# Optimization experiments

Measured on AMD Instinct MI355X. Metric: run time of the kernel, lower is better.

Reference implementation:

```python
import jax, jax.numpy as jnp
import numpy as np
from math import factorial

# ----- hyperparams (mirror init_kwargs) -----
HIDDEN = [(32,0,1),(32,0,-1),(8,1,1),(8,1,-1),(4,2,1),(4,2,-1)]  # (mul, l, parity)
SCALAR = [(32,0,1)]
SH_IRR = [(1,0,1),(1,1,-1),(1,2,1)]  # spherical harmonics 0e+1o+2e
EMB, NUM_RBF, R_MAX, MLP_DIM, D_IN = 32, 16, 10.0, 256, 64
N_NODES, N_EDGES, N_GRAPHS = 2048, 8192, 8
EDGE_FEATS_DIM = NUM_RBF + 2*EMB

def _slices(irs):
    s, o = [], 0
    for m, l, _ in irs:
        s.append(o); o += m*(2*l+1)
    return s

def _su2_cg(j1, j2, j3, m1, m2, m3):
    if m1 + m2 != m3:
        return 0.0
    f = factorial
    pref = ((2*j3+1)*f(j3+j1-j2)*f(j3-j1+j2)*f(j1+j2-j3)/f(j1+j2+j3+1))**0.5
    pref *= (f(j3+m3)*f(j3-m3)*f(j1-m1)*f(j1+m1)*f(j2-m2)*f(j2+m2))**0.5
    s = 0.0
    for k in range(0, j1+j2-j3+1):
        if j1-m1-k < 0 or j2+m2-k < 0 or j3-j2+m1+k < 0 or j3-j1-m2+k < 0:
            continue
        s += (-1.0)**k/(f(k)*f(j1+j2-j3-k)*f(j1-m1-k)*f(j2+m2-k)*f(j3-j2+m1+k)*f(j3-j1-m2+k))
    return pref*s

def _q(l):  # real -> complex change of basis (e3nn convention incl. (-i)^l phase)
    q = np.zeros((2*l+1, 2*l+1), dtype=np.complex128)
    for m in range(-l, 0):
        q[l+m, l+abs(m)] = 2**-0.5
        q[l+m, l-abs(m)] = -1j*2**-0.5
    q[l, l] = 1.0
    for m in range(1, l+1):
        q[l+m, l+abs(m)] = (-1)**m*2**-0.5
        q[l+m, l-abs(m)] = 1j*(-1)**m*2**-0.5
    return (-1j)**l*q

def _real_cg(l1, l2, l3):  # real-basis Clebsch-Gordan, unit Frobenius norm (wigner-3j-like)
    C = np.zeros((2*l1+1, 2*l2+1, 2*l3+1), dtype=np.complex128)
    for m1 in range(-l1, l1+1):
        for m2 in range(-l2, l2+1):
            m3 = m1 + m2
            if abs(m3) <= l3:
                C[l1+m1, l2+m2, l3+m3] = _su2_cg(l1, l2, l3, m1, m2, m3)
    w = np.einsum('ai,bj,ck,abc->ijk', _q(l1), _q(l2), np.conj(_q(l3)), C)
    re, im = np.real(w), np.imag(w)
    w = re if np.linalg.norm(re) >= np.linalg.norm(im) else im
    return (w/np.linalg.norm(w)).astype(np.float32)

_CG = {}
def cg(l1, l2, l3):
    if (l1, l2, l3) not in _CG:
        _CG[(l1, l2, l3)] = jnp.asarray(_real_cg(l1, l2, l3))
    return _CG[(l1, l2, l3)]

def _build_layer(ir_in, ir_out):  # FullyConnectedTensorProduct path enumeration
    si = _slices(ir_in)
    paths, woff, fan = [], 0, [0]*len(ir_out)
    for i1, (m1, l1, p1) in enumerate(ir_in):
        for (_, l2, p2) in SH_IRR:
            for i3, (m3, l3, p3) in enumerate(ir_out):
                if p1*p2 == p3 and abs(l1-l2) <= l3 <= l1+l2:
                    paths.append((si[i1], m1, l1, l2, i3, m3, l3, woff))
                    fan[i3] += m1
                    woff += m1*m3
    return paths, woff, fan, ir_out

L_SPECS = [_build_layer(SCALAR, HIDDEN), _build_layer(HIDDEN, HIDDEN),
           _build_layer(HIDDEN, HIDDEN), _build_layer(HIDDEN, SCALAR)]
W_NUMELS = [s[1] for s in L_SPECS]  # [1408, 4320, 4320, 1408]

def spherical_harmonics(u):  # component-normalized real SH, l=0,1,2, on unit vectors
    xc, yc, zc = u[:, 0], u[:, 1], u[:, 2]
    s3, s15, s5 = 3**0.5, 15**0.5, 5**0.5
    return jnp.stack([jnp.ones_like(xc),
                      s3*yc, s3*zc, s3*xc,
                      s15*xc*yc, s15*yc*zc, s5*0.5*(3*zc*zc-1.0), s15*xc*zc,
                      s15*0.5*(xc*xc-yc*yc)], axis=1)

def tp_messages(x, sh, w, spec):  # per-edge equivariant tensor product with edge-dep weights
    paths, _, fan, ir_out = spec
    E = x.shape[0]
    outs = [jnp.zeros((E, m*(2*l+1)), x.dtype) for m, l, _ in ir_out]
    for (o1, m1, l1, l2, i3, m3, l3, woff) in paths:
        xp = x[:, o1:o1+m1*(2*l1+1)].reshape(E, m1, 2*l1+1)
        shp = sh[:, l2*l2:(l2+1)*(l2+1)]
        wp = w[:, woff:woff+m1*m3].reshape(E, m1, m3)
        alpha = float(np.sqrt((2*l3+1)/fan[i3]))  # component/element path normalization
        y = alpha*jnp.einsum('eui,ej,euv,ijk->evk', xp, shp, wp, cg(l1, l2, l3))
        outs[i3] = outs[i3] + y.reshape(E, -1)
    return jnp.concatenate(outs, axis=1)

def batch_norm(h, ir_out, eps=1e-5):  # e3nn-style equivariant batch norm (train stats, identity affine)
    outs, o = [], 0
    for m, l, _ in ir_out:
        d = m*(2*l+1)
        f = h[:, o:o+d].reshape(-1, m, 2*l+1); o += d
        if l == 0:
            f = f - f.mean(axis=0, keepdims=True)
        norm2 = (f*f).mean(axis=(0, 2), keepdims=True)
        outs.append((f*jax.lax.rsqrt(norm2+eps)).reshape(h.shape[0], -1))
    return jnp.concatenate(outs, axis=1)

def scatter_mean(msg, idx, n):
    s = jax.ops.segment_sum(msg, idx, num_segments=n)
    c = jax.ops.segment_sum(jnp.ones((idx.shape[0], 1), msg.dtype), idx, num_segments=n)
    return s/jnp.maximum(c, 1.0)

def _forward(x, pos, edge_index, batch, emb_w, emb_b, layer_params):
    ei = jnp.concatenate([edge_index, edge_index[::-1]], axis=1)  # to_undirected (both directions)
    src, dst = ei[0], ei[1]
    h = x@emb_w + emb_b  # (N, 32)
    vec = pos[src] - pos[dst]
    lengths = jnp.linalg.norm(vec, axis=-1)
    sh = spherical_harmonics(vec/lengths[:, None])  # (E, 9)
    mu = jnp.linspace(0.0, R_MAX, NUM_RBF)
    sigma = R_MAX/NUM_RBF
    rbf = jnp.exp(-(((lengths[:, None]-mu)/sigma)**2))  # (E, 16)
    for li, (w1, b1, w2, b2) in enumerate(layer_params):
        ef = jnp.concatenate([rbf, h[src, :EMB], h[dst, :EMB]], axis=1)  # (E, 80)
        w = jax.nn.relu(ef@w1 + b1)@w2 + b2  # per-edge TP weights (dropout=eval noop)
        upd = scatter_mean(tp_messages(h[dst], sh, w, L_SPECS[li]), src, N_NODES)
        upd = batch_norm(upd, L_SPECS[li][3])
        d = upd.shape[-1]
        h_res = h[:, :d] if h.shape[-1] >= d else jnp.pad(h, ((0, 0), (0, d-h.shape[-1])))
        h = upd + h_res  # residual with pad/truncate (F.pad semantics)
    graph = jax.ops.segment_sum(h, batch, num_segments=N_GRAPHS)
    return h, graph

def setup_inputs():
    key = jax.random.key(0)
    ks = jax.random.split(key, 32)
    inp = {}
    inp['x'] = jax.random.normal(ks[0], (N_NODES, D_IN), jnp.float32)
    inp['pos'] = 3.0*jax.random.normal(ks[1], (N_NODES, 3), jnp.float32)
    s = jax.random.randint(ks[2], (N_EDGES,), 0, N_NODES)
    d = (s + jax.random.randint(ks[3], (N_EDGES,), 1, N_NODES)) % N_NODES  # no self-loops
    inp['edge_index'] = jnp.stack([s, d]).astype(jnp.int32)
    inp['batch'] = jnp.sort(jax.random.randint(ks[4], (N_NODES,), 0, N_GRAPHS)).astype(jnp.int32)
    inp['emb_w'] = jax.random.normal(ks[5], (D_IN, EMB), jnp.float32)/np.sqrt(D_IN)
    inp['emb_b'] = jnp.zeros((EMB,), jnp.float32)
    k = 6
    for i, wn in enumerate(W_NUMELS):
        inp[f'l{i}_w1'] = jax.random.normal(ks[k], (EDGE_FEATS_DIM, MLP_DIM), jnp.float32)/np.sqrt(EDGE_FEATS_DIM); k += 1
        inp[f'l{i}_b1'] = jnp.zeros((MLP_DIM,), jnp.float32)
        inp[f'l{i}_w2'] = jax.random.normal(ks[k], (MLP_DIM, wn), jnp.float32)/np.sqrt(MLP_DIM); k += 1
        inp[f'l{i}_b2'] = jnp.zeros((wn,), jnp.float32)
    return inp

def reference(x, pos, edge_index, batch, emb_w, emb_b,
              l0_w1, l0_b1, l0_w2, l0_b2, l1_w1, l1_b1, l1_w2, l1_b2,
              l2_w1, l2_b1, l2_w2, l2_b2, l3_w1, l3_b1, l3_w2, l3_b2):
    lp = [(l0_w1, l0_b1, l0_w2, l0_b2), (l1_w1, l1_b1, l1_w2, l1_b2),
          (l2_w1, l2_b1, l2_w2, l2_b2), (l3_w1, l3_b1, l3_w2, l3_b2)]
    return _forward(x, pos, edge_index, batch, emb_w, emb_b, lp)
```

## Files before the change

kernel.cpp:

```cpp
#include <hip/hip_runtime.h>
#include <hip/hip_bf16.h>
#include <math.h>

#define NNODES 2048
#define NEDG   8192
#define E2     16384
#define NGRAPH 8
#define HSTR   152

static const int LD_DIN[4]  = {32,152,152,152};
static const int LD_DOUT[4] = {152,152,152,32};
static const int LD_WN[4]   = {1408,4320,4320,1408};
static const int LD_WNP[4]  = {1408,4352,4352,1408};
static const int LD_NCH[4]  = {88,88,88,32};
static const int LD_RES[4]  = {32,152,152,152};
#define WNP_MAX 4352

#define SLOT_MAX    1088
#define CELL_N      20
#define SEG_S_N     164
#define SEG_ENT_MAX 1024

typedef short bf16x8 __attribute__((ext_vector_type(8)));
typedef float f32x4  __attribute__((ext_vector_type(4)));

constexpr double cfact(int n){ double r=1.0; for(int i=2;i<=n;i++) r*=(double)i; return r; }
constexpr double csqrt(double x){
  if(x<=0.0) return 0.0;
  double g = x>1.0? x:1.0;
  for(int i=0;i<64;i++) g=0.5*(g+x/g);
  return g;
}
constexpr double csu2cg(int j1,int j2,int j3,int m1,int m2,int m3){
  if(m1+m2!=m3) return 0.0;
  double pref = csqrt((double)(2*j3+1)*cfact(j3+j1-j2)*cfact(j3-j1+j2)*cfact(j1+j2-j3)/cfact(j1+j2+j3+1));
  pref *= csqrt(cfact(j3+m3)*cfact(j3-m3)*cfact(j1-m1)*cfact(j1+m1)*cfact(j2-m2)*cfact(j2+m2));
  double s=0.0;
  for(int k=0;k<=j1+j2-j3;k++){
    if(j1-m1-k<0||j2+m2-k<0||j3-j2+m1+k<0||j3-j1-m2+k<0) continue;
    double t=1.0/(cfact(k)*cfact(j1+j2-j3-k)*cfact(j1-m1-k)*cfact(j2+m2-k)*cfact(j3-j2+m1+k)*cfact(j3-j1-m2+k));
    s += (k&1)? -t : t;
  }
  return pref*s;
}
struct QM { double r[25]; double i[25]; };
constexpr QM cqmat(int l){
  QM q{};
  const double inv2=0.7071067811865476;
  for(int m=-l;m<0;m++){
    int am=-m;
    q.r[(l+m)*5+(l+am)] = inv2;
    q.i[(l+m)*5+(l-am)] = -inv2;
  }
  q.r[l*5+l]=1.0;
  for(int m=1;m<=l;m++){
    double sgn=(m&1)? -1.0:1.0;
    q.r[(l+m)*5+(l+m)] = sgn*inv2;
    q.i[(l+m)*5+(l-m)] = sgn*inv2;
  }
  for(int rep=0;rep<l;rep++){
    for(int t=0;t<25;t++){ double a=q.r[t], b=q.i[t]; q.r[t]=b; q.i[t]=-a; }
  }
  return q;
}
struct CGCell { float v[125]; };
constexpr CGCell mkcell(int l1,int l2,int l3){
  CGCell out{};
  int lo = l1>l2? l1-l2 : l2-l1;
  if(l3<lo || l3>l1+l2) return out;
  QM q1=cqmat(l1), q2=cqmat(l2), q3=cqmat(l3);
  int n1=2*l1+1,n2=2*l2+1,n3=2*l3+1;
  double C[125]={};
  for(int a=0;a<n1;a++)for(int b=0;b<n2;b++)for(int c=0;c<n3;c++)
    C[a*25+b*5+c]=csu2cg(l1,l2,l3,a-l1,b-l2,c-l3);
  double wr[125]={}, wi[125]={};
  for(int i=0;i<n1;i++)for(int j=0;j<n2;j++)for(int k=0;k<n3;k++){
    double ar=0.0, ai=0.0;
    for(int a=0;a<n1;a++)for(int b=0;b<n2;b++){
      double p1r=q1.r[a*5+i], p1i=q1.i[a*5+i];
      double p2r=q2.r[b*5+j], p2i=q2.i[b*5+j];
      double pr=p1r*p2r-p1i*p2i, pi=p1r*p2i+p1i*p2r;
      for(int c=0;c<n3;c++){
        double cv=C[a*25+b*5+c]; if(cv==0.0) continue;
        double p3r=q3.r[c*5+k], p3i=-q3.i[c*5+k];
        ar += (pr*p3r-pi*p3i)*cv;
        ai += (pr*p3i+pi*p3r)*cv;
      }
    }
    wr[i*25+j*5+k]=ar; wi[i*25+j*5+k]=ai;
  }
  double sr=0.0, si=0.0;
  for(int t=0;t<125;t++){ sr+=wr[t]*wr[t]; si+=wi[t]*wi[t]; }
  double nr=csqrt(sr), ni=csqrt(si);
  bool use_re = nr>=ni;
  double nn = use_re? nr:ni;
  double inv = (nn>1e-300)? 1.0/nn : 0.0;
  for(int t=0;t<125;t++) out.v[t]=(float)((use_re? wr[t]:wi[t])*inv);
  return out;
}
constexpr CGCell CGc0 =mkcell(0,0,0), CGc1 =mkcell(0,0,1), CGc2 =mkcell(0,0,2);
constexpr CGCell CGc3 =mkcell(0,1,0), CGc4 =mkcell(0,1,1), CGc5 =mkcell(0,1,2);
constexpr CGCell CGc6 =mkcell(0,2,0), CGc7 =mkcell(0,2,1), CGc8 =mkcell(0,2,2);
constexpr CGCell CGc9 =mkcell(1,0,0), CGc10=mkcell(1,0,1), CGc11=mkcell(1,0,2);
constexpr CGCell CGc12=mkcell(1,1,0), CGc13=mkcell(1,1,1), CGc14=mkcell(1,1,2);
constexpr CGCell CGc15=mkcell(1,2,0), CGc16=mkcell(1,2,1), CGc17=mkcell(1,2,2);
constexpr CGCell CGc18=mkcell(2,0,0), CGc19=mkcell(2,0,1), CGc20=mkcell(2,0,2);
constexpr CGCell CGc21=mkcell(2,1,0), CGc22=mkcell(2,1,1), CGc23=mkcell(2,1,2);
constexpr CGCell CGc24=mkcell(2,2,0), CGc25=mkcell(2,2,1), CGc26=mkcell(2,2,2);
__constant__ CGCell g_cg[27] = {
  CGc0,CGc1,CGc2,CGc3,CGc4,CGc5,CGc6,CGc7,CGc8,
  CGc9,CGc10,CGc11,CGc12,CGc13,CGc14,CGc15,CGc16,CGc17,
  CGc18,CGc19,CGc20,CGc21,CGc22,CGc23,CGc24,CGc25,CGc26};

#define MAXP 32
struct LayerSpec {
  int np, zc, wn, nc;
  int x_off[MAXP], m1[MAXP], d1[MAXP], sh_off[MAXP], d2[MAXP], d3[MAXP],
      m3[MAXP], woff[MAXP], out_sl[MAXP], cg_idx[MAXP], zbase[MAXP], cell[MAXP];
  float alpha[MAXP];
  int cellcg[16];
};
constexpr LayerSpec mkspec(int li){
  LayerSpec S{};
  const int IRH[6][3]={{32,0,1},{32,0,-1},{8,1,1},{8,1,-1},{4,2,1},{4,2,-1}};
  const int IRS[1][3]={{32,0,1}};
  const int SH2[3][2]={{0,1},{1,-1},{2,1}};
  const int (*irin)[3]  = (li==0)? IRS: IRH; int nin =(li==0)?1:6;
  const int (*irout)[3] = (li==3)? IRS: IRH; int nout=(li==3)?1:6;
  int si_in[6]={}, si_out[6]={};
  { int o=0; for(int i=0;i<nin;i++){ si_in[i]=o;  o+=irin[i][0]*(2*irin[i][1]+1);} }
  { int o=0; for(int i=0;i<nout;i++){ si_out[i]=o; o+=irout[i][0]*(2*irout[i][1]+1);} }
  int fan[6]={};
  int i3a[MAXP]={};
  int np=0, woff=0, zb=0, nc=0;
  for(int i1=0;i1<nin;i1++){
    int m1=irin[i1][0], l1=irin[i1][1], p1=irin[i1][2];
    for(int s=0;s<3;s++){
      int l2=SH2[s][0], p2=SH2[s][1];
      for(int i3=0;i3<nout;i3++){
        int m3=irout[i3][0], l3=irout[i3][1], p3=irout[i3][2];
        int lo = l1>l2? l1-l2 : l2-l1;
        if(p1*p2==p3 && l3>=lo && l3<=l1+l2){
          S.x_off[np]=si_in[i1]; S.m1[np]=m1; S.d1[np]=2*l1+1;
          S.sh_off[np]=l2*l2; S.d2[np]=2*l2+1; S.d3[np]=2*l3+1;
          S.m3[np]=m3; S.woff[np]=woff; S.out_sl[np]=si_out[i3];
          S.cg_idx[np]=l1*9+l2*3+l3; S.zbase[np]=zb;
          int ci=-1;
          for(int c=0;c<nc;c++) if(S.cellcg[c]==S.cg_idx[np]) ci=c;
          if(ci<0){ S.cellcg[nc]=S.cg_idx[np]; ci=nc++; }
          S.cell[np]=ci; i3a[np]=i3;
          np++;
          fan[i3]+=m1; woff+=m1*m3; zb+=m1*(2*l3+1);
        }
      }
    }
  }
  for(int p=0;p<np;p++)
    S.alpha[p]=(float)csqrt((double)(2*((S.d3[p]-1)/2)+1)/(double)fan[i3a[p]]);
  S.np=np; S.zc=zb; S.wn=woff; S.nc=nc;
  return S;
}
constexpr LayerSpec LS0=mkspec(0), LS1=mkspec(1), LS2=mkspec(2), LS3=mkspec(3);
__constant__ LayerSpec g_spec[4]={LS0,LS1,LS2,LS3};

__global__ __launch_bounds__(256) void build_tables_kernel(
    unsigned* __restrict__ slot_tab, unsigned* __restrict__ cell_tab,
    int* __restrict__ seg_start, unsigned* __restrict__ seg_ent,
    int* __restrict__ perm, float* __restrict__ alpha_col){
  __shared__ int vals[256];
  __shared__ int part[256];
  int tid=threadIdx.x;
  int li=blockIdx.x;
  const LayerSpec& S=g_spec[li];
  int np=S.np, zc=S.zc, nc=S.nc, wn=S.wn;
  for(int c=tid;c<nc;c+=256){
    int cgi=S.cellcg[c];
    int l2=(cgi/3)%3;
    cell_tab[li*CELL_N+c]=(unsigned)cgi | ((unsigned)(l2*l2)<<8) | ((unsigned)(2*l2+1)<<12);
  }
  for(int s=tid;s<zc;s+=256){
    int p=0; while(p+1<np && S.zbase[p+1]<=s) p++;
    int rel=s-S.zbase[p];
    int k=rel/S.m1[p], u=rel-k*S.m1[p];
    slot_tab[li*SLOT_MAX+s]=(unsigned)(S.x_off[p]+u*S.d1[p]) | ((unsigned)k<<9) | ((unsigned)S.cell[p]<<12);
  }
  int* pm=perm+li*WNP_MAX;
  float* ac=alpha_col+li*WNP_MAX;
  for(int j=tid;j<wn;j+=256){
    int p=0; while(p+1<np && S.woff[p+1]<=j) p++;
    int rel=j-S.woff[p];
    int v=rel/S.m1[p], u=rel%S.m1[p];
    pm[j]=S.woff[p]+u*S.m3[p]+v;
    ac[j]=S.alpha[p];
  }
  int Dout=(li==3)?32:152;
  for(int d=tid;d<Dout;d+=256){
    int cnt=0;
    for(int p=0;p<np;p++){
      int rel=d-S.out_sl[p];
      if(rel>=0 && rel<S.m3[p]*S.d3[p]) cnt++;
    }
    vals[d]=cnt;
  }
  __syncthreads();
  int v0=(tid<Dout)? vals[tid]:0;
  part[tid]=v0;
  __syncthreads();
  for(int ofs=1;ofs<256;ofs<<=1){
    int v=(tid>=ofs)? part[tid-ofs]:0;
    __syncthreads();
    part[tid]+=v;
    __syncthreads();
  }
  int* sst=seg_start+li*SEG_S_N;
  if(tid<Dout) sst[tid]=part[tid]-v0;
  if(tid==0) sst[Dout]=part[255];
  __syncthreads();
  unsigned* se=seg_ent+li*SEG_ENT_MAX;
  for(int d=tid;d<Dout;d+=256){
    int pos=sst[d];
    for(int p=0;p<np;p++){
      int rel=d-S.out_sl[p];
      if(rel>=0 && rel<S.m3[p]*S.d3[p]){
        int v=rel/S.d3[p], k=rel%S.d3[p];
        unsigned z0=(unsigned)(S.zbase[p]+k*S.m1[p]);
        unsigned w0=(unsigned)(S.woff[p]+v*S.m1[p]);
        unsigned code=(S.m1[p]==32)?2u:((S.m1[p]==8)?1u:0u);
        se[pos]= z0 | (w0<<11) | (code<<24);
        pos++;
      }
    }
  }
}

__global__ void geom_kernel(const float* __restrict__ pos, const int* __restrict__ ei,
                            int* __restrict__ src2, int* __restrict__ dst2,
                            float* __restrict__ sh, float* __restrict__ rbf,
                            int* __restrict__ counts){
  int e=blockIdx.x*256+threadIdx.x;
  if(e>=E2) return;
  int s,d;
  if(e<NEDG){ s=ei[e]; d=ei[NEDG+e]; }
  else { int j=e-NEDG; s=ei[NEDG+j]; d=ei[j]; }
  src2[e]=s; dst2[e]=d;
  atomicAdd(&counts[s],1);
  float vx=pos[s*3+0]-pos[d*3+0];
  float vy=pos[s*3+1]-pos[d*3+1];
  float vz=pos[s*3+2]-pos[d*3+2];
  float len=sqrtf(vx*vx+vy*vy+vz*vz);
  float inv=1.f/len;
  float x=vx*inv, y=vy*inv, z=vz*inv;
  const float s3=1.7320508075688772f, s15=3.872983346207417f, s5=2.23606797749979f;
  float* shp=sh+(size_t)e*9;
  shp[0]=1.f; shp[1]=s3*y; shp[2]=s3*z; shp[3]=s3*x;
  shp[4]=s15*x*y; shp[5]=s15*y*z; shp[6]=s5*0.5f*(3.f*z*z-1.f);
  shp[7]=s15*x*z; shp[8]=s15*0.5f*(x*x-y*y);
  float* rp=rbf+(size_t)e*16;
  const float invsig=1.6f;
  for(int k=0;k<16;k++){
    float t=(len-(10.0f/15.0f)*(float)k)*invsig;
    rp[k]=expf(-t*t);
  }
}

__global__ void invc_kernel(const int* __restrict__ counts, float* __restrict__ invc){
  int n=blockIdx.x*256+threadIdx.x;
  if(n>=NNODES) return;
  int c=counts[n]; if(c<1) c=1;
  invc[n]=1.f/(float)c;
}

__global__ void embed_kernel(const float* __restrict__ x, const float* __restrict__ W,
                             const float* __restrict__ b, float* __restrict__ h){
  int idx=blockIdx.x*256+threadIdx.x;
  int n=idx>>5, j=idx&31;
  float acc=b[j];
  for(int k=0;k<64;k++) acc += x[n*64+k]*W[k*32+j];
  h[(size_t)n*HSTR+j]=acc;
}

__global__ void cast_w2t_kernel(const float* __restrict__ w2, const int* __restrict__ perm,
                                const float* __restrict__ alpha_col,
                                __hip_bfloat16* __restrict__ w2t, int wn, int wn_pad){
  int idx=blockIdx.x*256+threadIdx.x;
  if(idx>=wn_pad*256) return;
  int j=idx>>8, k=idx&255;
  float v=(j<wn)? w2[(size_t)k*wn+perm[j]]*alpha_col[j] : 0.f;
  w2t[idx]=__float2bfloat16(v);
}

__global__ __launch_bounds__(256) void mlp1_kernel(
    const float* __restrict__ h, const float* __restrict__ rbf,
    const int* __restrict__ src2, const int* __restrict__ dst2,
    const float* __restrict__ w1, const float* __restrict__ b1,
    __hip_bfloat16* __restrict__ hidden, int e_start){
  __shared__ float ef[16][80];
  int tid=threadIdx.x;
  int e0=e_start+blockIdx.x*16;
  for(int t=tid;t<16*80;t+=256){
    int el=t/80, k=t-el*80; int ge=e0+el;
    float v;
    if(k<16)      v=rbf[(size_t)ge*16+k];
    else if(k<48) v=h[(size_t)src2[ge]*HSTR+(k-16)];
    else          v=h[(size_t)dst2[ge]*HSTR+(k-48)];
    ef[el][k]=v;
  }
  __syncthreads();
  float acc[16];
  float bv=b1[tid];
  #pragma unroll
  for(int e=0;e<16;e++) acc[e]=bv;
  for(int k=0;k<80;k++){
    float wv=w1[k*256+tid];
    #pragma unroll
    for(int e=0;e<16;e++) acc[e]+=ef[e][k]*wv;
  }
  int le0=blockIdx.x*16;
  #pragma unroll
  for(int e=0;e<16;e++)
    hidden[(size_t)(le0+e)*256+tid]=__float2bfloat16(fmaxf(acc[e],0.f));
}

__global__ __launch_bounds__(256) void mlp2_mfma_kernel(
    const __hip_bfloat16* __restrict__ hidden,
    const __hip_bfloat16* __restrict__ w2t,
    const float* __restrict__ b2, const int* __restrict__ perm,
    const float* __restrict__ alpha_col,
    __hip_bfloat16* __restrict__ wbuf, int wn, int wn_pad){
  __shared__ __hip_bfloat16 As[128*32];
  __shared__ __hip_bfloat16 Bs[128*32];
  int tid=threadIdx.x;
  int lane=tid&63;
  int m0=blockIdx.x*128, n0=blockIdx.y*128;
  int mw=((tid>>6)&1)*64, nw=(tid>>7)*64;
  f32x4 acc[4][4];
  #pragma unroll
  for(int i=0;i<4;i++)
    #pragma unroll
    for(int j=0;j<4;j++) acc[i][j]=(f32x4){0.f,0.f,0.f,0.f};

  int i0=tid*8, i1=tid*8+2048;
  int ar0=i0>>5, ac0=i0&31, ar1=i1>>5, ac1=i1&31;
  const int q4=lane>>4, c16=lane&15;

  for(int k0=0;k0<256;k0+=32){
    __syncthreads();
    *(uint4*)&As[ar0*32+ac0] = *(const uint4*)&hidden[(size_t)(m0+ar0)*256 + k0 + ac0];
    *(uint4*)&As[ar1*32+ac1] = *(const uint4*)&hidden[(size_t)(m0+ar1)*256 + k0 + ac1];
    *(uint4*)&Bs[ar0*32+ac0] = *(const uint4*)&w2t[(size_t)(n0+ar0)*256 + k0 + ac0];
    *(uint4*)&Bs[ar1*32+ac1] = *(const uint4*)&w2t[(size_t)(n0+ar1)*256 + k0 + ac1];
    __syncthreads();
    bf16x8 af[4], bfr[4];
    #pragma unroll
    for(int mi=0;mi<4;mi++) af[mi]=*(bf16x8*)&As[(mw+mi*16+c16)*32 + q4*8];
    #pragma unroll
    for(int ni=0;ni<4;ni++) bfr[ni]=*(bf16x8*)&Bs[(nw+ni*16+c16)*32 + q4*8];
    #pragma unroll
    for(int mi=0;mi<4;mi++)
      #pragma unroll
      for(int ni=0;ni<4;ni++)
        acc[mi][ni]=__builtin_amdgcn_mfma_f32_16x16x32_bf16(af[mi],bfr[ni],acc[mi][ni],0,0,0);
  }
  #pragma unroll
  for(int ni=0;ni<4;ni++){
    int col=n0+nw+ni*16+c16;
    float bias=(col<wn)? b2[perm[col]]*alpha_col[col]:0.f;
    #pragma unroll
    for(int mi=0;mi<4;mi++){
      int row=m0+mw+mi*16+q4*4;
      #pragma unroll
      for(int rr=0;rr<4;rr++)
        wbuf[(size_t)(row+rr)*wn_pad+col]=__float2bfloat16(acc[mi][ni][rr]+bias);
    }
  }
}

__device__ inline void wave_sync(){
  __builtin_amdgcn_s_waitcnt(0);
  __builtin_amdgcn_wave_barrier();
}

__device__ inline float dot4z(const __hip_bfloat16* zp, const __hip_bfloat16* wp){
  uint2 zv=*(const uint2*)zp;
  uint2 wv=*(const uint2*)wp;
  const __hip_bfloat16* zl=(const __hip_bfloat16*)&zv;
  const __hip_bfloat16* wl=(const __hip_bfloat16*)&wv;
  float s=0.f;
  #pragma unroll
  for(int q=0;q<4;q++) s+=__bfloat162float(zl[q])*__bfloat162float(wl[q]);
  return s;
}
__device__ inline float dot8z(const __hip_bfloat16* zp, const __hip_bfloat16* wp){
  return dot4z(zp,wp)+dot4z(zp+4,wp+4);
}

__global__ __launch_bounds__(256) void tp4_kernel(
    const float* __restrict__ h, const float* __restrict__ sh,
    const __hip_bfloat16* __restrict__ wbuf,
    const int* __restrict__ src2, const int* __restrict__ dst2,
    const unsigned* __restrict__ slot_tab, const unsigned* __restrict__ cell_tab,
    const int* __restrict__ seg_start, const unsigned* __restrict__ seg_ent,
    float* __restrict__ upd, int e_start, int Din, int Dout, int wstride,
    int zc, int nc){
  __shared__ float xrow[4][160];
  __shared__ float shs[4][12];
  __shared__ __hip_bfloat16 zsm[4][1088];
  __shared__ float Tw[4][376];
  int tid=threadIdx.x, w=tid>>6, lane=tid&63;
  int le=blockIdx.x*4+w, ge=e_start+le;
  int dn=dst2[ge];
  int sn=src2[ge];
  for(int i=lane;i<Din;i+=64) xrow[w][i]=h[(size_t)dn*HSTR+i];
  for(int i=Din+lane;i<160;i+=64) xrow[w][i]=0.f;
  if(lane<9) shs[w][lane]=sh[(size_t)ge*9+lane];
  wave_sync();
  float* T=&Tw[w][0];
  for(int t=lane;t<nc*25;t+=64){
    int c=t/25, r=t-c*25, k=r/5, i=r-k*5;
    unsigned cm=cell_tab[c];
    int cgi=cm&255, sho=(cm>>8)&15, d2=(cm>>12)&7;
    const float* cgp=g_cg[cgi].v + i*25 + k;
    float s=0.f;
    for(int j=0;j<d2;j++) s+=cgp[j*5]*shs[w][sho+j];
    T[t]=s;
  }
  wave_sync();
  const float* xr=&xrow[w][0];
  for(int s=lane;s<zc;s+=64){
    unsigned st=slot_tab[s];
    int xb=st&511, k=(st>>9)&7, c=st>>12;
    const float* Tp=&T[c*25+k*5];
    float v=xr[xb]*Tp[0]+xr[xb+1]*Tp[1]+xr[xb+2]*Tp[2]+xr[xb+3]*Tp[3]+xr[xb+4]*Tp[4];
    zsm[w][s]=__float2bfloat16(v);
  }
  wave_sync();
  const __hip_bfloat16* wrow=wbuf+(size_t)le*wstride;
  const __hip_bfloat16* zbase=&zsm[w][0];
  float* urow=upd+(size_t)sn*Dout;
  for(int d=lane;d<Dout;d+=64){
    int s0=seg_start[d], s1=seg_start[d+1];
    float acc=0.f;
    for(int s=s0;s<s1;s++){
      unsigned sg=seg_ent[s];
      int z0=sg&2047, w0=(sg>>11)&8191, code=sg>>24;
      const __hip_bfloat16* zp=zbase+z0;
      const __hip_bfloat16* wp=wrow+w0;
      if(code==2){
        #pragma unroll
        for(int t=0;t<4;t++) acc+=dot8z(zp+t*8,wp+t*8);
      } else if(code==1){
        acc+=dot8z(zp,wp);
      } else {
        acc+=dot4z(zp,wp);
      }
    }
    atomicAdd(&urow[d], acc);
  }
}

__device__ inline int hidden_chan_of_dim(int d){
  if(d<64)  return d;
  if(d<88)  return 64+(d-64)/3;
  if(d<112) return 72+(d-88)/3;
  if(d<132) return 80+(d-112)/5;
  return 84+(d-132)/5;
}
__device__ inline void hidden_chan_params(int c, int& off, int& dk, int& l0){
  if(c<64){ off=c; dk=1; l0=1; }
  else if(c<72){ off=64+(c-64)*3; dk=3; l0=0; }
  else if(c<80){ off=88+(c-72)*3; dk=3; l0=0; }
  else if(c<84){ off=112+(c-80)*5; dk=5; l0=0; }
  else { off=132+(c-84)*5; dk=5; l0=0; }
}

__global__ void stats_kernel(const float* __restrict__ upd, const float* __restrict__ invc,
                             float* __restrict__ stats, int Dout, int scalar_out){
  int c=blockIdx.x, tid=threadIdx.x;
  int off,dk,l0;
  if(scalar_out){ off=c; dk=1; l0=1; }
  else hidden_chan_params(c,off,dk,l0);
  float s=0.f, s2=0.f;
  int total=NNODES*dk;
  for(int t=tid;t<total;t+=256){
    int n=t/dk, k=t-n*dk;
    float v=upd[(size_t)n*Dout+off+k]*invc[n];
    s+=v; s2+=v*v;
  }
  __shared__ float rs[256], rs2[256];
  rs[tid]=s; rs2[tid]=s2; __syncthreads();
  for(int o=128;o>0;o>>=1){
    if(tid<o){ rs[tid]+=rs[tid+o]; rs2[tid]+=rs2[tid+o]; }
    __syncthreads();
  }
  if(tid==0){
    float cnt=(float)total;
    float mean = l0? rs[0]/cnt : 0.f;
    float var = rs2[0]/cnt - mean*mean;
    stats[c*2]=mean;
    stats[c*2+1]=1.0f/sqrtf(var+1e-5f);
  }
}

__global__ void apply_kernel(const float* __restrict__ upd, const float* __restrict__ invc,
                             const float* __restrict__ stats,
                             const float* __restrict__ h_cur, float* __restrict__ h_next,
                             int Dout, int res_dim, int scalar_out, int out_stride){
  int idx=blockIdx.x*256+threadIdx.x;
  if(idx>=NNODES*Dout) return;
  int n=idx/Dout, d=idx-n*Dout;
  int c = scalar_out? d : hidden_chan_of_dim(d);
  float v=(upd[idx]*invc[n]-stats[2*c])*stats[2*c+1];
  float res=(d<res_dim)? h_cur[(size_t)n*HSTR+d] : 0.f;
  h_next[(size_t)n*out_stride+d]=v+res;
}

__global__ void graph_kernel(const float* __restrict__ hfin, const int* __restrict__ batch,
                             float* __restrict__ gout){
  int idx=blockIdx.x*256+threadIdx.x;
  int n=idx>>5, d=idx&31;
  atomicAdd(&gout[batch[n]*32+d], hfin[idx]);
}

extern "C" void kernel_launch(void* const* d_in, const int* in_sizes, int n_in,
                              void* d_out, int out_size, void* d_ws, size_t ws_size,
                              hipStream_t stream){
  (void)in_sizes; (void)n_in; (void)out_size;
  const float* x    =(const float*)d_in[0];
  const float* pos  =(const float*)d_in[1];
  const int*   ei   =(const int*)d_in[2];
  const int*   batch=(const int*)d_in[3];
  const float* emb_w=(const float*)d_in[4];
  const float* emb_b=(const float*)d_in[5];
  const float *W1[4], *B1[4], *W2[4], *B2[4];
  for(int l=0;l<4;l++){
    W1[l]=(const float*)d_in[6+4*l];
    B1[l]=(const float*)d_in[7+4*l];
    W2[l]=(const float*)d_in[8+4*l];
    B2[l]=(const float*)d_in[9+4*l];
  }
  int ZC[4]={LS0.zc,LS1.zc,LS2.zc,LS3.zc};
  int NC[4]={LS0.nc,LS1.nc,LS2.nc,LS3.nc};

  char* base=(char*)d_ws;
  size_t off=0;
  auto alloc=[&](size_t bytes)->char*{
    off=(off+255)&~(size_t)255;
    char* p=base+off; off+=bytes; return p;
  };
  float*  h_a   =(float*)alloc((size_t)NNODES*HSTR*4);
  float*  h_b   =(float*)alloc((size_t)NNODES*HSTR*4);
  float*  shb   =(float*)alloc((size_t)E2*9*4);
  float*  rbfb  =(float*)alloc((size_t)E2*16*4);
  int*    src2  =(int*)  alloc((size_t)E2*4);
  int*    dst2  =(int*)  alloc((size_t)E2*4);
  int*    counts=(int*)  alloc((size_t)NNODES*4);
  float*  invc  =(float*)alloc((size_t)NNODES*4);
  float*  upd   =(float*)alloc((size_t)NNODES*HSTR*4);
  float*  stats =(float*)alloc(256*4);
  unsigned* slot_tab=(unsigned*)alloc((size_t)4*SLOT_MAX*4);
  unsigned* cell_tg =(unsigned*)alloc((size_t)4*CELL_N*4);
  int*      seg_s   =(int*)     alloc((size_t)4*SEG_S_N*4);
  unsigned* seg_e   =(unsigned*)alloc((size_t)4*SEG_ENT_MAX*4);
  int*      perm    =(int*)     alloc((size_t)4*WNP_MAX*4);
  float*    alpha_c =(float*)   alloc((size_t)4*WNP_MAX*4);
  __hip_bfloat16* w2t[4];
  for(int l=0;l<4;l++) w2t[l]=(__hip_bfloat16*)alloc((size_t)LD_WNP[l]*256*2);

  int E_CHUNK=E2;
  while(E_CHUNK>128){
    size_t need=off;
    need=(need+255)&~(size_t)255; need+=(size_t)E_CHUNK*256*2;
    need=(need+255)&~(size_t)255; need+=(size_t)E_CHUNK*WNP_MAX*2;
    if(need<=ws_size) break;
    E_CHUNK>>=1;
  }
  __hip_bfloat16* hidden=(__hip_bfloat16*)alloc((size_t)E_CHUNK*256*2);
  __hip_bfloat16* wbuf  =(__hip_bfloat16*)alloc((size_t)E_CHUNK*WNP_MAX*2);

  hipMemsetAsync(counts,0,(size_t)NNODES*4,stream);
  build_tables_kernel<<<4,256,0,stream>>>(slot_tab,cell_tg,seg_s,seg_e,perm,alpha_c);
  geom_kernel<<<E2/256,256,0,stream>>>(pos,ei,src2,dst2,shb,rbfb,counts);
  invc_kernel<<<NNODES/256,256,0,stream>>>(counts,invc);
  embed_kernel<<<(NNODES*32)/256,256,0,stream>>>(x,emb_w,emb_b,h_a);
  for(int l=0;l<4;l++)
    cast_w2t_kernel<<<(LD_WNP[l]*256+255)/256,256,0,stream>>>(
        W2[l],perm+l*WNP_MAX,alpha_c+l*WNP_MAX,w2t[l],LD_WN[l],LD_WNP[l]);

  float* h_cur=h_a; float* h_nxt=h_b;
  for(int li=0;li<4;li++){
    int wn=LD_WN[li], wnp=LD_WNP[li], Din=LD_DIN[li], Dout=LD_DOUT[li];
    hipMemsetAsync(upd,0,(size_t)NNODES*Dout*4,stream);
    for(int e0=0;e0<E2;e0+=E_CHUNK){
      mlp1_kernel<<<E_CHUNK/16,256,0,stream>>>(h_cur,rbfb,src2,dst2,W1[li],B1[li],hidden,e0);
      dim3 g2(E_CHUNK/128, wnp/128);
      mlp2_mfma_kernel<<<g2,256,0,stream>>>(hidden,w2t[li],B2[li],perm+li*WNP_MAX,
                                            alpha_c+li*WNP_MAX,wbuf,wn,wnp);
      tp4_kernel<<<E_CHUNK/4,256,0,stream>>>(h_cur,shb,wbuf,src2,dst2,
          slot_tab+li*SLOT_MAX, cell_tg+li*CELL_N,
          seg_s+li*SEG_S_N, seg_e+li*SEG_ENT_MAX,
          upd,e0,Din,Dout,wnp, ZC[li], NC[li]);
    }
    stats_kernel<<<LD_NCH[li],256,0,stream>>>(upd,invc,stats,Dout,li==3?1:0);
    int tot=NNODES*Dout;
    if(li<3)
      apply_kernel<<<(tot+255)/256,256,0,stream>>>(upd,invc,stats,h_cur,h_nxt,Dout,LD_RES[li],0,HSTR);
    else
      apply_kernel<<<(tot+255)/256,256,0,stream>>>(upd,invc,stats,h_cur,(float*)d_out,Dout,LD_RES[li],1,32);
    float* tmp=h_cur; h_cur=h_nxt; h_nxt=tmp;
  }

  float* gout=(float*)d_out + (size_t)NNODES*32;
  hipMemsetAsync(gout,0,(size_t)NGRAPH*32*4,stream);
  graph_kernel<<<(NNODES*32)/256,256,0,stream>>>((const float*)d_out,batch,gout);
}
```

Baseline: 731.2 us.

## Merge weight casts, fold memsets into apply, prefetch tables in tensor-product kernel

```diff
diff --git a/kernel.cpp b/kernel.cpp
--- a/kernel.cpp
+++ b/kernel.cpp
@@ -15,6 +15,7 @@
 static const int LD_NCH[4]  = {88,88,88,32};
 static const int LD_RES[4]  = {32,152,152,152};
 #define WNP_MAX 4352
+#define WNP_TOT (1408+4352+4352+1408)
 
 #define SLOT_MAX    1088
 #define CELL_N      20
@@ -279,14 +280,27 @@
   h[(size_t)n*HSTR+j]=acc;
 }
 
-__global__ void cast_w2t_kernel(const float* __restrict__ w2, const int* __restrict__ perm,
-                                const float* __restrict__ alpha_col,
-                                __hip_bfloat16* __restrict__ w2t, int wn, int wn_pad){
+__global__ void cast_all_kernel(const float* __restrict__ w2_0, const float* __restrict__ w2_1,
+                                const float* __restrict__ w2_2, const float* __restrict__ w2_3,
+                                const int* __restrict__ perm, const float* __restrict__ alpha_col,
+                                __hip_bfloat16* __restrict__ w2t_all){
   int idx=blockIdx.x*256+threadIdx.x;
-  if(idx>=wn_pad*256) return;
-  int j=idx>>8, k=idx&255;
-  float v=(j<wn)? w2[(size_t)k*wn+perm[j]]*alpha_col[j] : 0.f;
-  w2t[idx]=__float2bfloat16(v);
+  if(idx>=WNP_TOT*256) return;
+  int jj=idx>>8, k=idx&255;
+  int l, j0;
+  if(jj<1408){ l=0; j0=0; }
+  else if(jj<1408+4352){ l=1; j0=1408; }
+  else if(jj<1408+4352+4352){ l=2; j0=1408+4352; }
+  else { l=3; j0=1408+4352+4352; }
+  int j=jj-j0;
+  const float* w2 = (l==0)? w2_0 : (l==1)? w2_1 : (l==2)? w2_2 : w2_3;
+  int wn=LD_WN[l];
+  float v=0.f;
+  if(j<wn){
+    int pj=perm[l*WNP_MAX+j];
+    v=w2[(size_t)k*wn+pj]*alpha_col[l*WNP_MAX+j];
+  }
+  w2t_all[idx]=__float2bfloat16(v);
 }
 
 __global__ __launch_bounds__(256) void mlp1_kernel(
@@ -392,6 +406,24 @@
 }
 __device__ inline float dot8z(const __hip_bfloat16* zp, const __hip_bfloat16* wp){
   return dot4z(zp,wp)+dot4z(zp+4,wp+4);
+}
+
+__device__ inline float seg_dot(unsigned sg, const __hip_bfloat16* zbase,
+                                const __hip_bfloat16* wrow){
+  int z0=sg&2047, w0=(sg>>11)&8191, code=sg>>24;
+  const __hip_bfloat16* zp=zbase+z0;
+  const __hip_bfloat16* wp=wrow+w0;
+  float s;
+  if(code==2){
+    s=0.f;
+    #pragma unroll
+    for(int t=0;t<4;t++) s+=dot8z(zp+t*8,wp+t*8);
+  } else if(code==1){
+    s=dot8z(zp,wp);
+  } else {
+    s=dot4z(zp,wp);
+  }
+  return s;
 }
 
 __global__ __launch_bounds__(256) void tp4_kernel(
@@ -426,8 +458,11 @@
   }
   wave_sync();
   const float* xr=&xrow[w][0];
+  unsigned st_next = slot_tab[lane];
   for(int s=lane;s<zc;s+=64){
-    unsigned st=slot_tab[s];
+    unsigned st=st_next;
+    int s2=s+64;
+    if(s2<zc) st_next=slot_tab[s2];
     int xb=st&511, k=(st>>9)&7, c=st>>12;
     const float* Tp=&T[c*25+k*5];
     float v=xr[xb]*Tp[0]+xr[xb+1]*Tp[1]+xr[xb+2]*Tp[2]+xr[xb+3]*Tp[3]+xr[xb+4]*Tp[4];
@@ -439,22 +474,20 @@
   float* urow=upd+(size_t)sn*Dout;
   for(int d=lane;d<Dout;d+=64){
     int s0=seg_start[d], s1=seg_start[d+1];
-    float acc=0.f;
-    for(int s=s0;s<s1;s++){
-      unsigned sg=seg_ent[s];
-      int z0=sg&2047, w0=(sg>>11)&8191, code=sg>>24;
-      const __hip_bfloat16* zp=zbase+z0;
-      const __hip_bfloat16* wp=wrow+w0;
-      if(code==2){
-        #pragma unroll
-        for(int t=0;t<4;t++) acc+=dot8z(zp+t*8,wp+t*8);
-      } else if(code==1){
-        acc+=dot8z(zp,wp);
-      } else {
-        acc+=dot4z(zp,wp);
-      }
+    int ns=s1-s0;
+    unsigned sgs[8];
+    int npre=ns>8?8:ns;
+    #pragma unroll 8
+    for(int i=0;i<npre;i++) sgs[i]=seg_ent[s0+i];
+    float a0=0.f, a1=0.f;
+    int i=0;
+    for(; i+1<npre; i+=2){
+      a0+=seg_dot(sgs[i],   zbase, wrow);
+      a1+=seg_dot(sgs[i+1], zbase, wrow);
     }
-    atomicAdd(&urow[d], acc);
+    if(i<npre) a0+=seg_dot(sgs[i], zbase, wrow);
+    for(int j=8;j<ns;j++) a1+=seg_dot(seg_ent[s0+j], zbase, wrow);
+    atomicAdd(&urow[d], a0+a1);
   }
 }
 
@@ -501,17 +534,21 @@
   }
 }
 
-__global__ void apply_kernel(const float* __restrict__ upd, const float* __restrict__ invc,
+__global__ void apply_kernel(float* __restrict__ upd, const float* __restrict__ invc,
                              const float* __restrict__ stats,
                              const float* __restrict__ h_cur, float* __restrict__ h_next,
+                             float* __restrict__ gout_zero,
                              int Dout, int res_dim, int scalar_out, int out_stride){
   int idx=blockIdx.x*256+threadIdx.x;
   if(idx>=NNODES*Dout) return;
   int n=idx/Dout, d=idx-n*Dout;
   int c = scalar_out? d : hidden_chan_of_dim(d);
-  float v=(upd[idx]*invc[n]-stats[2*c])*stats[2*c+1];
+  float uv=upd[idx];
+  upd[idx]=0.f;
+  float v=(uv*invc[n]-stats[2*c])*stats[2*c+1];
   float res=(d<res_dim)? h_cur[(size_t)n*HSTR+d] : 0.f;
   h_next[(size_t)n*out_stride+d]=v+res;
+  if(gout_zero && idx<NGRAPH*32) gout_zero[idx]=0.f;
 }
 
 __global__ void graph_kernel(const float* __restrict__ hfin, const int* __restrict__ batch,
@@ -540,6 +577,7 @@
   }
   int ZC[4]={LS0.zc,LS1.zc,LS2.zc,LS3.zc};
   int NC[4]={LS0.nc,LS1.nc,LS2.nc,LS3.nc};
+  const int W2TOFF[4]={0,1408,1408+4352,1408+4352+4352};
 
   char* base=(char*)d_ws;
   size_t off=0;
@@ -563,8 +601,7 @@
   unsigned* seg_e   =(unsigned*)alloc((size_t)4*SEG_ENT_MAX*4);
   int*      perm    =(int*)     alloc((size_t)4*WNP_MAX*4);
   float*    alpha_c =(float*)   alloc((size_t)4*WNP_MAX*4);
-  __hip_bfloat16* w2t[4];
-  for(int l=0;l<4;l++) w2t[l]=(__hip_bfloat16*)alloc((size_t)LD_WNP[l]*256*2);
+  __hip_bfloat16* w2t_all=(__hip_bfloat16*)alloc((size_t)WNP_TOT*256*2);
 
   int E_CHUNK=E2;
   while(E_CHUNK>128){
@@ -578,22 +615,21 @@
   __hip_bfloat16* wbuf  =(__hip_bfloat16*)alloc((size_t)E_CHUNK*WNP_MAX*2);
 
   hipMemsetAsync(counts,0,(size_t)NNODES*4,stream);
+  hipMemsetAsync(upd,0,(size_t)NNODES*HSTR*4,stream);
   build_tables_kernel<<<4,256,0,stream>>>(slot_tab,cell_tg,seg_s,seg_e,perm,alpha_c);
   geom_kernel<<<E2/256,256,0,stream>>>(pos,ei,src2,dst2,shb,rbfb,counts);
   invc_kernel<<<NNODES/256,256,0,stream>>>(counts,invc);
   embed_kernel<<<(NNODES*32)/256,256,0,stream>>>(x,emb_w,emb_b,h_a);
-  for(int l=0;l<4;l++)
-    cast_w2t_kernel<<<(LD_WNP[l]*256+255)/256,256,0,stream>>>(
-        W2[l],perm+l*WNP_MAX,alpha_c+l*WNP_MAX,w2t[l],LD_WN[l],LD_WNP[l]);
+  cast_all_kernel<<<(WNP_TOT*256)/256,256,0,stream>>>(W2[0],W2[1],W2[2],W2[3],perm,alpha_c,w2t_all);
 
   float* h_cur=h_a; float* h_nxt=h_b;
   for(int li=0;li<4;li++){
     int wn=LD_WN[li], wnp=LD_WNP[li], Din=LD_DIN[li], Dout=LD_DOUT[li];
-    hipMemsetAsync(upd,0,(size_t)NNODES*Dout*4,stream);
+    __hip_bfloat16* w2t=w2t_all+(size_t)W2TOFF[li]*256;
     for(int e0=0;e0<E2;e0+=E_CHUNK){
       mlp1_kernel<<<E_CHUNK/16,256,0,stream>>>(h_cur,rbfb,src2,dst2,W1[li],B1[li],hidden,e0);
       dim3 g2(E_CHUNK/128, wnp/128);
-      mlp2_mfma_kernel<<<g2,256,0,stream>>>(hidden,w2t[li],B2[li],perm+li*WNP_MAX,
+      mlp2_mfma_kernel<<<g2,256,0,stream>>>(hidden,w2t,B2[li],perm+li*WNP_MAX,
                                             alpha_c+li*WNP_MAX,wbuf,wn,wnp);
       tp4_kernel<<<E_CHUNK/4,256,0,stream>>>(h_cur,shb,wbuf,src2,dst2,
           slot_tab+li*SLOT_MAX, cell_tg+li*CELL_N,
@@ -603,13 +639,15 @@
     stats_kernel<<<LD_NCH[li],256,0,stream>>>(upd,invc,stats,Dout,li==3?1:0);
     int tot=NNODES*Dout;
     if(li<3)
-      apply_kernel<<<(tot+255)/256,256,0,stream>>>(upd,invc,stats,h_cur,h_nxt,Dout,LD_RES[li],0,HSTR);
+      apply_kernel<<<(tot+255)/256,256,0,stream>>>(upd,invc,stats,h_cur,h_nxt,
+                                                   (float*)nullptr,Dout,LD_RES[li],0,HSTR);
     else
-      apply_kernel<<<(tot+255)/256,256,0,stream>>>(upd,invc,stats,h_cur,(float*)d_out,Dout,LD_RES[li],1,32);
+      apply_kernel<<<(tot+255)/256,256,0,stream>>>(upd,invc,stats,h_cur,(float*)d_out,
+                                                   (float*)d_out+(size_t)NNODES*32,
+                                                   Dout,LD_RES[li],1,32);
     float* tmp=h_cur; h_cur=h_nxt; h_nxt=tmp;
   }
 
   float* gout=(float*)d_out + (size_t)NNODES*32;
-  hipMemsetAsync(gout,0,(size_t)NGRAPH*32*4,stream);
   graph_kernel<<<(NNODES*32)/256,256,0,stream>>>((const float*)d_out,batch,gout);
 }
```

Result: slower. 753.1 us (+3.0%).
